# Kernel tuning notes

Hardware: AMD Instinct MI355X
Metric: run time of the kernel (lower is better)

The kernel has to match this reference:

```python
import jax, jax.numpy as jnp
import numpy as np

HEADS = 16
EPS = 1e-5  # torch LayerNorm default


def _ln(x, s, b):
    m = jnp.mean(x, axis=-1, keepdims=True)
    v = jnp.mean((x - m) ** 2, axis=-1, keepdims=True)
    return (x - m) * jax.lax.rsqrt(v + EPS) * s + b


def setup_inputs() -> dict:
    key = jax.random.key(0)
    B, N, D, DEPTH, MLP = 2, 1024, 1024, 6, 4096
    ks = jax.random.split(key, 6)
    s = 0.02  # init scale so activations stay well-conditioned
    return {
        "x": jax.random.normal(ks[0], (B, N, D), dtype=jnp.float32),
        "ln1_s": jnp.ones((DEPTH, D), jnp.float32),
        "ln1_b": jnp.zeros((DEPTH, D), jnp.float32),
        "w_qkv": jax.random.normal(ks[1], (DEPTH, D, 3 * D), dtype=jnp.float32) * s,
        "w_out": jax.random.normal(ks[2], (DEPTH, D, D), dtype=jnp.float32) * s,
        "b_out": jnp.zeros((DEPTH, D), jnp.float32),
        "ln2_s": jnp.ones((DEPTH, D), jnp.float32),
        "ln2_b": jnp.zeros((DEPTH, D), jnp.float32),
        "w1": jax.random.normal(ks[3], (DEPTH, D, MLP), dtype=jnp.float32) * s,
        "b1": jnp.zeros((DEPTH, MLP), jnp.float32),
        "w2": jax.random.normal(ks[4], (DEPTH, MLP, D), dtype=jnp.float32) * s,
        "b2": jnp.zeros((DEPTH, D), jnp.float32),
    }


def reference(x, ln1_s, ln1_b, w_qkv, w_out, b_out, ln2_s, ln2_b, w1, b1, w2, b2):
    D = x.shape[-1]
    dh = D // HEADS
    scale = D ** -0.5  # NOTE: original scales by full dim**-0.5, not head_dim

    def layer(xc, p):
        l1s, l1b, wq, wo, bo, l2s, l2b, W1, B1, W2, B2 = p
        h = _ln(xc, l1s, l1b)
        b, n, _ = h.shape
        qkv = (h @ wq).reshape(b, n, 3, HEADS, dh)  # 'b n (qkv h d)' split order
        q = qkv[:, :, 0].transpose(0, 2, 1, 3)  # bhnd
        k = qkv[:, :, 1].transpose(0, 2, 1, 3)
        v = qkv[:, :, 2].transpose(0, 2, 1, 3)
        dots = jnp.einsum('bhid,bhjd->bhij', q, k) * scale
        attn = jax.nn.softmax(dots, axis=-1)
        o = jnp.einsum('bhij,bhjd->bhid', attn, v)
        o = o.transpose(0, 2, 1, 3).reshape(b, n, D)
        xc = xc + (o @ wo + bo)  # Residual(PreNorm(Attention))
        h2 = _ln(xc, l2s, l2b)
        xc = xc + (jax.nn.gelu(h2 @ W1 + B1, approximate=False) @ W2 + B2)
        return xc, None

    x, _ = jax.lax.scan(layer, x, (ln1_s, ln1_b, w_qkv, w_out, b_out,
                                   ln2_s, ln2_b, w1, b1, w2, b2))
    return x
```

## Files before the change

### kernel.cpp

```cpp
#include <hip/hip_runtime.h>
#include <math.h>

typedef unsigned short ushort_t;
typedef __bf16 bf16x8 __attribute__((ext_vector_type(8)));
typedef float f32x4 __attribute__((ext_vector_type(4)));

#define HEADS 16

__device__ __forceinline__ ushort_t f2b(float f) {
    unsigned int u = __float_as_uint(f);
    unsigned int r = (u + 0x7FFFu + ((u >> 16) & 1u)) >> 16;
    return (ushort_t)r;
}

__device__ __forceinline__ void g2lds(const void* g, void* l) {
    __builtin_amdgcn_global_load_lds(
        (const __attribute__((address_space(1))) unsigned int*)g,
        (__attribute__((address_space(3))) unsigned int*)l, 16, 0, 0);
}

__global__ __launch_bounds__(256) void copy_kernel(const float* __restrict__ x,
                                                   float* __restrict__ y) {
    int i = blockIdx.x * 256 + threadIdx.x;
    ((float4*)y)[i] = ((const float4*)x)[i];
}

__global__ __launch_bounds__(256) void transpose_kernel(const float* __restrict__ W,
                                                        ushort_t* __restrict__ Wt,
                                                        int K, int N) {
    __shared__ ushort_t sT[64 * 72];
    const int t = threadIdx.x;
    const int k0 = blockIdx.y * 64;
    const int n0 = blockIdx.x * 64;
    const int kk = t >> 4;
    const int nc = (t & 15) * 4;
#pragma unroll
    for (int i = 0; i < 4; i++) {
        int k = kk + i * 16;
        float4 v = *(const float4*)(W + (size_t)(k0 + k) * N + n0 + nc);
        const float* vf = (const float*)&v;
#pragma unroll
        for (int j = 0; j < 4; j++) sT[(nc + j) * 72 + k] = f2b(vf[j]);
    }
    __syncthreads();
#pragma unroll
    for (int p = 0; p < 2; p++) {
        int u = t + p * 256;
        int n = u >> 3;
        int kc = (u & 7) * 8;
        *(uint4*)(Wt + (size_t)(n0 + n) * K + k0 + kc) = *(const uint4*)(sT + n * 72 + kc);
    }
}

__global__ __launch_bounds__(256) void ln_kernel(const float* __restrict__ x,
                                                 const float* __restrict__ s,
                                                 const float* __restrict__ b,
                                                 ushort_t* __restrict__ out) {
    int row = blockIdx.x;
    int t = threadIdx.x;
    const float* xr = x + (size_t)row * 1024;
    float4 xv = *(const float4*)(xr + t * 4);
    float sum = xv.x + xv.y + xv.z + xv.w;
    float sq = xv.x * xv.x + xv.y * xv.y + xv.z * xv.z + xv.w * xv.w;
#pragma unroll
    for (int m = 1; m < 64; m <<= 1) {
        sum += __shfl_xor(sum, m);
        sq += __shfl_xor(sq, m);
    }
    __shared__ float red[8];
    int wave = t >> 6, lane = t & 63;
    if (lane == 0) { red[wave] = sum; red[4 + wave] = sq; }
    __syncthreads();
    sum = red[0] + red[1] + red[2] + red[3];
    sq = red[4] + red[5] + red[6] + red[7];
    float mean = sum * (1.0f / 1024.0f);
    float var = sq * (1.0f / 1024.0f) - mean * mean;
    float inv = rsqrtf(var + 1e-5f);
    float4 sv = *(const float4*)(s + t * 4);
    float4 bv = *(const float4*)(b + t * 4);
    unsigned int lo = (unsigned int)f2b((xv.x - mean) * inv * sv.x + bv.x) |
                      ((unsigned int)f2b((xv.y - mean) * inv * sv.y + bv.y) << 16);
    unsigned int hi = (unsigned int)f2b((xv.z - mean) * inv * sv.z + bv.z) |
                      ((unsigned int)f2b((xv.w - mean) * inv * sv.w + bv.w) << 16);
    uint2 o;
    o.x = lo; o.y = hi;
    *(uint2*)(out + (size_t)row * 1024 + t * 4) = o;
}

template <int MODE>
__global__ __launch_bounds__(256) void gemm_bt_kernel(
    const ushort_t* __restrict__ A, const ushort_t* __restrict__ Bt,
    const float* __restrict__ bias, float* __restrict__ res,
    ushort_t* __restrict__ outb, ushort_t* __restrict__ qo,
    ushort_t* __restrict__ ko, ushort_t* __restrict__ vto, int K, int N) {
    __shared__ __align__(16) ushort_t sA[3][64 * 64];
    __shared__ __align__(16) ushort_t sB[3][64 * 64];
    const int t = threadIdx.x;
    const int lane = t & 63;
    const int wave = t >> 6;
    const int l15 = lane & 15;
    const int quad = lane >> 4;
    const int wm = wave >> 1, wn = wave & 1;

    const int gx = gridDim.x, gy = gridDim.y;
    const int nwg = gx * gy;
    const int L = blockIdx.x + gx * blockIdx.y;
    const int f = (L & 7) * (nwg >> 3) + (L >> 3);
    const int bx = f % gx;
    const int by = f / gx;

    const int m0 = by * 64;
    const int n0 = bx * 64;

    f32x4 acc[2][2];
#pragma unroll
    for (int i = 0; i < 2; i++)
#pragma unroll
        for (int j = 0; j < 2; j++) acc[i][j] = (f32x4){0.f, 0.f, 0.f, 0.f};

    const int rlow = lane >> 3;
    const int chunk = (lane & 7) ^ rlow;
    const int rowS = wave * 8 + rlow;
    const ushort_t* gA = A + (size_t)(m0 + rowS) * K + chunk * 8;
    const ushort_t* gB = Bt + (size_t)(n0 + rowS) * K + chunk * 8;
    const int lslot = wave * 512;
    const int xorv = l15 & 7;

    const int nkt = K >> 6;
#pragma unroll
    for (int b2 = 0; b2 < 2; b2++) {
#pragma unroll
        for (int p = 0; p < 2; p++) {
            g2lds(gA + (size_t)p * 32 * K + b2 * 64, &sA[b2][0] + lslot + p * 2048);
            g2lds(gB + (size_t)p * 32 * K + b2 * 64, &sB[b2][0] + lslot + p * 2048);
        }
    }

    int cur = 0;
    for (int kt = 0; kt < nkt; kt++) {
        if (kt + 1 < nkt)
            asm volatile("s_waitcnt vmcnt(4)" ::: "memory");
        else
            asm volatile("s_waitcnt vmcnt(0)" ::: "memory");
        __builtin_amdgcn_sched_barrier(0);
        __builtin_amdgcn_s_barrier();
        __builtin_amdgcn_sched_barrier(0);
        if (kt + 2 < nkt) {
            const size_t koff = (size_t)(kt + 2) * 64;
            const int nb = cur >= 1 ? cur - 1 : 2;
            ushort_t* dA = &sA[nb][0] + lslot;
            ushort_t* dB = &sB[nb][0] + lslot;
#pragma unroll
            for (int p = 0; p < 2; p++) {
                g2lds(gA + (size_t)p * 32 * K + koff, dA + p * 2048);
                g2lds(gB + (size_t)p * 32 * K + koff, dB + p * 2048);
            }
        }
        const ushort_t* cA = &sA[cur][0];
        const ushort_t* cB = &sB[cur][0];
#pragma unroll
        for (int ks = 0; ks < 2; ks++) {
            const int co = ((ks * 4 + quad) ^ xorv) * 8;
            bf16x8 af[2], bf[2];
#pragma unroll
            for (int i = 0; i < 2; i++)
                af[i] = *(const bf16x8*)(cA + (wm * 32 + i * 16 + l15) * 64 + co);
#pragma unroll
            for (int i = 0; i < 2; i++)
                bf[i] = *(const bf16x8*)(cB + (wn * 32 + i * 16 + l15) * 64 + co);
#pragma unroll
            for (int mi = 0; mi < 2; mi++)
#pragma unroll
                for (int ni = 0; ni < 2; ni++)
                    acc[mi][ni] = __builtin_amdgcn_mfma_f32_16x16x32_bf16(
                        af[mi], bf[ni], acc[mi][ni], 0, 0, 0);
        }
        __builtin_amdgcn_sched_barrier(0);
        cur = cur == 2 ? 0 : cur + 1;
    }
#pragma unroll
    for (int mi = 0; mi < 2; mi++) {
#pragma unroll
        for (int ni = 0; ni < 2; ni++) {
#pragma unroll
            for (int r = 0; r < 4; r++) {
                int mg = m0 + wm * 32 + mi * 16 + quad * 4 + r;
                int ng = n0 + wn * 32 + ni * 16 + l15;
                float c = acc[mi][ni][r];
                if (MODE == 1) {
                    size_t idx = (size_t)mg * N + ng;
                    res[idx] = res[idx] + c + bias[ng];
                } else if (MODE == 2) {
                    float vv = c + bias[ng];
                    float g = 0.5f * vv * (1.0f + erff(vv * 0.70710678118654752f));
                    outb[(size_t)mg * N + ng] = f2b(g);
                } else {
                    int qkv = ng >> 10;
                    int rem = ng & 1023;
                    int hh = rem >> 6;
                    int dd = rem & 63;
                    int bb = mg >> 10;
                    int seq = mg & 1023;
                    ushort_t val = f2b(c);
                    if (qkv == 0)
                        qo[((size_t)(bb * HEADS + hh) * 1024 + seq) * 64 + dd] = val;
                    else if (qkv == 1)
                        ko[((size_t)(bb * HEADS + hh) * 1024 + seq) * 64 + dd] = val;
                    else
                        vto[((size_t)(bb * HEADS + hh) * 64 + dd) * 1024 + seq] = val;
                }
            }
        }
    }
}

__global__ __launch_bounds__(256) void attn_kernel(const ushort_t* __restrict__ q,
                                                   const ushort_t* __restrict__ k,
                                                   const ushort_t* __restrict__ vt,
                                                   ushort_t* __restrict__ o) {
    __shared__ __align__(16) ushort_t sK[64 * 72];
    __shared__ __align__(16) ushort_t sV[64 * 72];
    __shared__ __align__(16) ushort_t sP[4 * 16 * 72];
    const int t = threadIdx.x;
    const int lane = t & 63;
    const int w = t >> 6;
    const int l15 = lane & 15;
    const int quad = lane >> 4;
    const int L = blockIdx.x + 16 * blockIdx.y;
    const int f = (L & 7) * 64 + (L >> 3);
    const int qt = f & 15;
    const int bh = f >> 4;

    bf16x8 aq[2];
    const ushort_t* qbase = q + ((size_t)bh * 1024 + qt * 64 + w * 16 + l15) * 64;
    aq[0] = *(const bf16x8*)(qbase + quad * 8);
    aq[1] = *(const bf16x8*)(qbase + 32 + quad * 8);

    float m_old[4], l_sum[4];
    f32x4 oacc[4];
#pragma unroll
    for (int r = 0; r < 4; r++) { m_old[r] = -1e30f; l_sum[r] = 0.f; }
#pragma unroll
    for (int i = 0; i < 4; i++) oacc[i] = (f32x4){0.f, 0.f, 0.f, 0.f};

    const float scale = 0.03125f;

    for (int kt = 0; kt < 16; kt++) {
        __syncthreads();
#pragma unroll
        for (int p = 0; p < 2; p++) {
            int u = t + p * 256;
            int row = u >> 3, ch = u & 7;
            uint4 v = *(const uint4*)(k + ((size_t)bh * 1024 + kt * 64 + row) * 64 + ch * 8);
            *(uint4*)(sK + row * 72 + ch * 8) = v;
            uint4 v2 = *(const uint4*)(vt + ((size_t)bh * 64 + row) * 1024 + kt * 64 + ch * 8);
            *(uint4*)(sV + row * 72 + ch * 8) = v2;
        }
        __syncthreads();
        f32x4 s[4];
#pragma unroll
        for (int nt = 0; nt < 4; nt++) {
            f32x4 a = (f32x4){0.f, 0.f, 0.f, 0.f};
#pragma unroll
            for (int ks = 0; ks < 2; ks++) {
                bf16x8 bk = *(const bf16x8*)(sK + (nt * 16 + l15) * 72 + ks * 32 + quad * 8);
                a = __builtin_amdgcn_mfma_f32_16x16x32_bf16(aq[ks], bk, a, 0, 0, 0);
            }
            s[nt] = a * scale;
        }
        float alpha[4];
#pragma unroll
        for (int r = 0; r < 4; r++) {
            float mx = fmaxf(fmaxf(s[0][r], s[1][r]), fmaxf(s[2][r], s[3][r]));
#pragma unroll
            for (int msk = 1; msk < 16; msk <<= 1) mx = fmaxf(mx, __shfl_xor(mx, msk));
            float mnew = fmaxf(m_old[r], mx);
            alpha[r] = __expf(m_old[r] - mnew);
            float psum = 0.f;
#pragma unroll
            for (int nt = 0; nt < 4; nt++) {
                float p = __expf(s[nt][r] - mnew);
                s[nt][r] = p;
                psum += p;
            }
#pragma unroll
            for (int msk = 1; msk < 16; msk <<= 1) psum += __shfl_xor(psum, msk);
            l_sum[r] = l_sum[r] * alpha[r] + psum;
            m_old[r] = mnew;
        }
#pragma unroll
        for (int i = 0; i < 4; i++)
#pragma unroll
            for (int r = 0; r < 4; r++) oacc[i][r] *= alpha[r];
#pragma unroll
        for (int nt = 0; nt < 4; nt++)
#pragma unroll
            for (int r = 0; r < 4; r++)
                sP[w * 1152 + (quad * 4 + r) * 72 + nt * 16 + l15] = f2b(s[nt][r]);
        __syncthreads();
#pragma unroll
        for (int nt = 0; nt < 4; nt++) {
#pragma unroll
            for (int ks = 0; ks < 2; ks++) {
                bf16x8 ap = *(const bf16x8*)(sP + w * 1152 + l15 * 72 + ks * 32 + quad * 8);
                bf16x8 bv = *(const bf16x8*)(sV + (nt * 16 + l15) * 72 + ks * 32 + quad * 8);
                oacc[nt] = __builtin_amdgcn_mfma_f32_16x16x32_bf16(ap, bv, oacc[nt], 0, 0, 0);
            }
        }
    }
    int b = bh >> 4, hh = bh & 15;
#pragma unroll
    for (int nt = 0; nt < 4; nt++)
#pragma unroll
        for (int r = 0; r < 4; r++) {
            int row = qt * 64 + w * 16 + quad * 4 + r;
            float val = oacc[nt][r] / l_sum[r];
            o[((size_t)b * 1024 + row) * 1024 + hh * 64 + nt * 16 + l15] = f2b(val);
        }
}

extern "C" void kernel_launch(void* const* d_in, const int* in_sizes, int n_in,
                              void* d_out, int out_size, void* d_ws, size_t ws_size,
                              hipStream_t stream) {
    const float* x = (const float*)d_in[0];
    const float* ln1_s = (const float*)d_in[1];
    const float* ln1_b = (const float*)d_in[2];
    const float* w_qkv = (const float*)d_in[3];
    const float* w_out = (const float*)d_in[4];
    const float* b_out = (const float*)d_in[5];
    const float* ln2_s = (const float*)d_in[6];
    const float* ln2_b = (const float*)d_in[7];
    const float* w1 = (const float*)d_in[8];
    const float* b1 = (const float*)d_in[9];
    const float* w2 = (const float*)d_in[10];
    const float* b2 = (const float*)d_in[11];

    float* res = (float*)d_out;
    char* wsb = (char*)d_ws;
    const size_t MB = 1024 * 1024;
    ushort_t* h = (ushort_t*)(wsb + 0 * MB);
    ushort_t* qb = (ushort_t*)(wsb + 4 * MB);
    ushort_t* kb = (ushort_t*)(wsb + 8 * MB);
    ushort_t* vtb = (ushort_t*)(wsb + 12 * MB);
    ushort_t* ob = (ushort_t*)(wsb + 16 * MB);
    ushort_t* ub = (ushort_t*)(wsb + 4 * MB);
    ushort_t* wqkv_t = (ushort_t*)(wsb + 20 * MB);
    ushort_t* wo_t = (ushort_t*)(wsb + 26 * MB);
    ushort_t* w12_t = (ushort_t*)(wsb + 20 * MB);

    copy_kernel<<<2048, 256, 0, stream>>>(x, res);
    for (int l = 0; l < 6; l++) {
        transpose_kernel<<<dim3(48, 16), 256, 0, stream>>>(
            w_qkv + (size_t)l * 1024 * 3072, wqkv_t, 1024, 3072);
        transpose_kernel<<<dim3(16, 16), 256, 0, stream>>>(
            w_out + (size_t)l * 1024 * 1024, wo_t, 1024, 1024);
        ln_kernel<<<2048, 256, 0, stream>>>(res, ln1_s + l * 1024, ln1_b + l * 1024, h);
        gemm_bt_kernel<0><<<dim3(48, 32), 256, 0, stream>>>(
            h, wqkv_t, nullptr, nullptr, nullptr, qb, kb, vtb, 1024, 3072);
        attn_kernel<<<dim3(16, 32), 256, 0, stream>>>(qb, kb, vtb, ob);
        gemm_bt_kernel<1><<<dim3(16, 32), 256, 0, stream>>>(
            ob, wo_t, b_out + l * 1024, res, nullptr, nullptr, nullptr, nullptr,
            1024, 1024);
        transpose_kernel<<<dim3(64, 16), 256, 0, stream>>>(
            w1 + (size_t)l * 1024 * 4096, w12_t, 1024, 4096);
        ln_kernel<<<2048, 256, 0, stream>>>(res, ln2_s + l * 1024, ln2_b + l * 1024, h);
        gemm_bt_kernel<2><<<dim3(64, 32), 256, 0, stream>>>(
            h, w12_t, b1 + l * 4096, nullptr, ub, nullptr, nullptr, nullptr,
            1024, 4096);
        transpose_kernel<<<dim3(16, 64), 256, 0, stream>>>(
            w2 + (size_t)l * 4096 * 1024, w12_t, 4096, 1024);
        gemm_bt_kernel<1><<<dim3(16, 32), 256, 0, stream>>>(
            ub, w12_t, b2 + l * 1024, res, nullptr, nullptr, nullptr, nullptr,
            4096, 1024);
    }
}
```

Baseline: 1.477 ms.

## Split-K the residual GEMMs and fold partial sums into LayerNorm

The two N=1024 residual GEMMs (out-projection and MLP down-projection) now split K across a grid z-dimension when workspace allows. Only z=0 updates the residual; the other slices write fp32 partials that the next LayerNorm kernel, or a final reduce kernel, adds back in. This doubles the block count on these 512-tile GEMMs to improve CU occupancy, at the cost of extra partial-buffer traffic. Separately, the attention kernel now prefetches the next K/V tile into registers while the current tile is stored to LDS.

```diff
diff --git a/kernel.cpp b/kernel.cpp
--- a/kernel.cpp
+++ b/kernel.cpp
@@ -6,6 +6,7 @@
 typedef float f32x4 __attribute__((ext_vector_type(4)));
 
 #define HEADS 16
+#define RES_ELEMS ((size_t)2048 * 1024)
 
 __device__ __forceinline__ ushort_t f2b(float f) {
     unsigned int u = __float_as_uint(f);
@@ -52,14 +53,20 @@
     }
 }
 
-__global__ __launch_bounds__(256) void ln_kernel(const float* __restrict__ x,
+__global__ __launch_bounds__(256) void ln_kernel(float* __restrict__ x,
+                                                 const float* __restrict__ part, int np,
                                                  const float* __restrict__ s,
                                                  const float* __restrict__ b,
                                                  ushort_t* __restrict__ out) {
     int row = blockIdx.x;
     int t = threadIdx.x;
-    const float* xr = x + (size_t)row * 1024;
-    float4 xv = *(const float4*)(xr + t * 4);
+    size_t off = (size_t)row * 1024 + t * 4;
+    float4 xv = *(const float4*)(x + off);
+    for (int p = 0; p < np; p++) {
+        float4 pv = *(const float4*)(part + (size_t)p * RES_ELEMS + off);
+        xv.x += pv.x; xv.y += pv.y; xv.z += pv.z; xv.w += pv.w;
+    }
+    if (np > 0) *(float4*)(x + off) = xv;
     float sum = xv.x + xv.y + xv.z + xv.w;
     float sq = xv.x * xv.x + xv.y * xv.y + xv.z * xv.z + xv.w * xv.w;
 #pragma unroll
@@ -87,10 +94,22 @@
     *(uint2*)(out + (size_t)row * 1024 + t * 4) = o;
 }
 
+__global__ __launch_bounds__(256) void reduce_kernel(float* __restrict__ res,
+                                                     const float* __restrict__ part, int np) {
+    size_t i = ((size_t)blockIdx.x * 256 + threadIdx.x) * 4;
+    float4 a = *(const float4*)(res + i);
+    for (int p = 0; p < np; p++) {
+        float4 pv = *(const float4*)(part + (size_t)p * RES_ELEMS + i);
+        a.x += pv.x; a.y += pv.y; a.z += pv.z; a.w += pv.w;
+    }
+    *(float4*)(res + i) = a;
+}
+
 template <int MODE>
 __global__ __launch_bounds__(256) void gemm_bt_kernel(
     const ushort_t* __restrict__ A, const ushort_t* __restrict__ Bt,
     const float* __restrict__ bias, float* __restrict__ res,
+    float* __restrict__ part,
     ushort_t* __restrict__ outb, ushort_t* __restrict__ qo,
     ushort_t* __restrict__ ko, ushort_t* __restrict__ vto, int K, int N) {
     __shared__ __align__(16) ushort_t sA[3][64 * 64];
@@ -102,15 +121,19 @@
     const int quad = lane >> 4;
     const int wm = wave >> 1, wn = wave & 1;
 
-    const int gx = gridDim.x, gy = gridDim.y;
-    const int nwg = gx * gy;
-    const int L = blockIdx.x + gx * blockIdx.y;
+    const int gx = gridDim.x, gy = gridDim.y, gz = gridDim.z;
+    const int nwg = gx * gy * gz;
+    const int L = blockIdx.x + gx * (blockIdx.y + gy * blockIdx.z);
     const int f = (L & 7) * (nwg >> 3) + (L >> 3);
     const int bx = f % gx;
-    const int by = f / gx;
+    const int rem = f / gx;
+    const int by = rem % gy;
+    const int bz = rem / gy;
 
     const int m0 = by * 64;
     const int n0 = bx * 64;
+    const int Ks = K / gz;
+    const int kbeg = bz * Ks;
 
     f32x4 acc[2][2];
 #pragma unroll
@@ -121,12 +144,12 @@
     const int rlow = lane >> 3;
     const int chunk = (lane & 7) ^ rlow;
     const int rowS = wave * 8 + rlow;
-    const ushort_t* gA = A + (size_t)(m0 + rowS) * K + chunk * 8;
-    const ushort_t* gB = Bt + (size_t)(n0 + rowS) * K + chunk * 8;
+    const ushort_t* gA = A + (size_t)(m0 + rowS) * K + kbeg + chunk * 8;
+    const ushort_t* gB = Bt + (size_t)(n0 + rowS) * K + kbeg + chunk * 8;
     const int lslot = wave * 512;
     const int xorv = l15 & 7;
 
-    const int nkt = K >> 6;
+    const int nkt = Ks >> 6;
 #pragma unroll
     for (int b2 = 0; b2 < 2; b2++) {
 #pragma unroll
@@ -189,16 +212,19 @@
                 float c = acc[mi][ni][r];
                 if (MODE == 1) {
                     size_t idx = (size_t)mg * N + ng;
-                    res[idx] = res[idx] + c + bias[ng];
+                    if (bz == 0)
+                        res[idx] = res[idx] + c + bias[ng];
+                    else
+                        part[(size_t)(bz - 1) * RES_ELEMS + idx] = c;
                 } else if (MODE == 2) {
                     float vv = c + bias[ng];
                     float g = 0.5f * vv * (1.0f + erff(vv * 0.70710678118654752f));
                     outb[(size_t)mg * N + ng] = f2b(g);
                 } else {
                     int qkv = ng >> 10;
-                    int rem = ng & 1023;
-                    int hh = rem >> 6;
-                    int dd = rem & 63;
+                    int rem2 = ng & 1023;
+                    int hh = rem2 >> 6;
+                    int dd = rem2 & 63;
                     int bb = mg >> 10;
                     int seq = mg & 1023;
                     ushort_t val = f2b(c);
@@ -245,16 +271,31 @@
 
     const float scale = 0.03125f;
 
+    const int row0 = t >> 3, ch0 = (t & 7) * 8;
+    const int row1 = (t + 256) >> 3;
+    uint4 rK[2], rV[2];
+#pragma unroll
+    for (int p = 0; p < 2; p++) {
+        int row = p == 0 ? row0 : row1;
+        rK[p] = *(const uint4*)(k + ((size_t)bh * 1024 + row) * 64 + ch0);
+        rV[p] = *(const uint4*)(vt + ((size_t)bh * 64 + row) * 1024 + ch0);
+    }
+
     for (int kt = 0; kt < 16; kt++) {
         __syncthreads();
 #pragma unroll
         for (int p = 0; p < 2; p++) {
-            int u = t + p * 256;
-            int row = u >> 3, ch = u & 7;
-            uint4 v = *(const uint4*)(k + ((size_t)bh * 1024 + kt * 64 + row) * 64 + ch * 8);
-            *(uint4*)(sK + row * 72 + ch * 8) = v;
-            uint4 v2 = *(const uint4*)(vt + ((size_t)bh * 64 + row) * 1024 + kt * 64 + ch * 8);
-            *(uint4*)(sV + row * 72 + ch * 8) = v2;
+            int row = p == 0 ? row0 : row1;
+            *(uint4*)(sK + row * 72 + ch0) = rK[p];
+            *(uint4*)(sV + row * 72 + ch0) = rV[p];
+        }
+        if (kt + 1 < 16) {
+#pragma unroll
+            for (int p = 0; p < 2; p++) {
+                int row = p == 0 ? row0 : row1;
+                rK[p] = *(const uint4*)(k + ((size_t)bh * 1024 + (kt + 1) * 64 + row) * 64 + ch0);
+                rV[p] = *(const uint4*)(vt + ((size_t)bh * 64 + row) * 1024 + (kt + 1) * 64 + ch0);
+            }
         }
         __syncthreads();
         f32x4 s[4];
@@ -348,29 +389,36 @@
     ushort_t* wo_t = (ushort_t*)(wsb + 26 * MB);
     ushort_t* w12_t = (ushort_t*)(wsb + 20 * MB);
 
+    int zs = (ws_size >= 44 * MB) ? 2 : 1;
+    float* part_wo = (float*)(wsb + 28 * MB);
+    float* part_ml = (float*)(wsb + 36 * MB);
+
     copy_kernel<<<2048, 256, 0, stream>>>(x, res);
     for (int l = 0; l < 6; l++) {
         transpose_kernel<<<dim3(48, 16), 256, 0, stream>>>(
             w_qkv + (size_t)l * 1024 * 3072, wqkv_t, 1024, 3072);
         transpose_kernel<<<dim3(16, 16), 256, 0, stream>>>(
             w_out + (size_t)l * 1024 * 1024, wo_t, 1024, 1024);
-        ln_kernel<<<2048, 256, 0, stream>>>(res, ln1_s + l * 1024, ln1_b + l * 1024, h);
-        gemm_bt_kernel<0><<<dim3(48, 32), 256, 0, stream>>>(
-            h, wqkv_t, nullptr, nullptr, nullptr, qb, kb, vtb, 1024, 3072);
+        ln_kernel<<<2048, 256, 0, stream>>>(res, part_ml, l == 0 ? 0 : zs - 1,
+                                            ln1_s + l * 1024, ln1_b + l * 1024, h);
+        gemm_bt_kernel<0><<<dim3(48, 32, 1), 256, 0, stream>>>(
+            h, wqkv_t, nullptr, nullptr, nullptr, nullptr, qb, kb, vtb, 1024, 3072);
         attn_kernel<<<dim3(16, 32), 256, 0, stream>>>(qb, kb, vtb, ob);
-        gemm_bt_kernel<1><<<dim3(16, 32), 256, 0, stream>>>(
-            ob, wo_t, b_out + l * 1024, res, nullptr, nullptr, nullptr, nullptr,
+        gemm_bt_kernel<1><<<dim3(16, 32, zs), 256, 0, stream>>>(
+            ob, wo_t, b_out + l * 1024, res, part_wo, nullptr, nullptr, nullptr, nullptr,
             1024, 1024);
         transpose_kernel<<<dim3(64, 16), 256, 0, stream>>>(
             w1 + (size_t)l * 1024 * 4096, w12_t, 1024, 4096);
-        ln_kernel<<<2048, 256, 0, stream>>>(res, ln2_s + l * 1024, ln2_b + l * 1024, h);
-        gemm_bt_kernel<2><<<dim3(64, 32), 256, 0, stream>>>(
-            h, w12_t, b1 + l * 4096, nullptr, ub, nullptr, nullptr, nullptr,
+        ln_kernel<<<2048, 256, 0, stream>>>(res, part_wo, zs - 1,
+                                            ln2_s + l * 1024, ln2_b + l * 1024, h);
+        gemm_bt_kernel<2><<<dim3(64, 32, 1), 256, 0, stream>>>(
+            h, w12_t, b1 + l * 4096, nullptr, nullptr, ub, nullptr, nullptr, nullptr,
             1024, 4096);
         transpose_kernel<<<dim3(16, 64), 256, 0, stream>>>(
             w2 + (size_t)l * 4096 * 1024, w12_t, 4096, 1024);
-        gemm_bt_kernel<1><<<dim3(16, 32), 256, 0, stream>>>(
-            ub, w12_t, b2 + l * 1024, res, nullptr, nullptr, nullptr, nullptr,
+        gemm_bt_kernel<1><<<dim3(16, 32, zs), 256, 0, stream>>>(
+            ub, w12_t, b2 + l * 1024, res, part_ml, nullptr, nullptr, nullptr, nullptr,
             4096, 1024);
     }
-}
+    if (zs > 1) reduce_kernel<<<2048, 256, 0, stream>>>(res, part_ml, zs - 1);
+}
```

Measured after the change: 1.631 ms. 1.1x slower.
